# Optimization experiments

Measured on AMD Instinct MI355X. Metric: run time of the kernel, lower is better.

## Reference

```python
import jax, jax.numpy as jnp
import numpy as np

B, S, IN, H, OUT, L = 64, 2048, 208, 100, 98, 2


def setup_inputs() -> dict:
    key = jax.random.key(0)
    ks = jax.random.split(key, 11)
    sc = 1.0 / np.sqrt(H)  # pytorch GRU init scale
    return {
        "sequence": jax.random.normal(ks[0], (B, S, IN), jnp.float32),
        "h0": jnp.zeros((L, B, H), jnp.float32),
        "w_ih_l0": jax.random.normal(ks[1], (3 * H, IN), jnp.float32) * sc,
        "w_hh_l0": jax.random.normal(ks[2], (3 * H, H), jnp.float32) * sc,
        "b_ih_l0": jax.random.normal(ks[3], (3 * H,), jnp.float32) * sc,
        "b_hh_l0": jax.random.normal(ks[4], (3 * H,), jnp.float32) * sc,
        "w_ih_l1": jax.random.normal(ks[5], (3 * H, H), jnp.float32) * sc,
        "w_hh_l1": jax.random.normal(ks[6], (3 * H, H), jnp.float32) * sc,
        "b_ih_l1": jax.random.normal(ks[7], (3 * H,), jnp.float32) * sc,
        "b_hh_l1": jax.random.normal(ks[8], (3 * H,), jnp.float32) * sc,
        "w_out": jax.random.normal(ks[9], (OUT, H), jnp.float32) * sc,
        "b_out": jax.random.normal(ks[10], (OUT,), jnp.float32) * sc,
    }


def _gru_layer(x, h0, w_ih, w_hh, b_ih, b_hh):
    # x: (B,S,Din), h0: (B,H). PyTorch GRU gate order: r, z, n.
    Hd = h0.shape[-1]
    xg = jnp.einsum("bsi,gi->bsg", x, w_ih) + b_ih  # (B,S,3H) input projections, batched GEMM

    def step(h, xg_t):
        hg = h @ w_hh.T + b_hh  # (B,3H)
        xr, xz, xn = xg_t[:, :Hd], xg_t[:, Hd:2 * Hd], xg_t[:, 2 * Hd:]
        hr, hz, hn = hg[:, :Hd], hg[:, Hd:2 * Hd], hg[:, 2 * Hd:]
        r = jax.nn.sigmoid(xr + hr)
        z = jax.nn.sigmoid(xz + hz)
        n = jnp.tanh(xn + r * hn)
        h_new = (1.0 - z) * n + z * h
        return h_new, h_new

    h_last, ys = jax.lax.scan(step, h0, jnp.swapaxes(xg, 0, 1))  # scan over time
    return jnp.swapaxes(ys, 0, 1), h_last  # (B,S,H)


def reference(sequence, h0, w_ih_l0, w_hh_l0, b_ih_l0, b_hh_l0,
              w_ih_l1, w_hh_l1, b_ih_l1, b_hh_l1, w_out, b_out):
    # 2-layer unidirectional GRU (eval mode: inter-layer dropout inactive) + linear head
    y0, _ = _gru_layer(sequence, h0[0], w_ih_l0, w_hh_l0, b_ih_l0, b_hh_l0)
    y1, _ = _gru_layer(y0, h0[1], w_ih_l1, w_hh_l1, b_ih_l1, b_hh_l1)
    return jnp.einsum("bsh,oh->bso", y1, w_out) + b_out  # (B,S,OUT)
```

## Files before the change

kernel.cpp:

```cpp
#include <hip/hip_runtime.h>


#define GB_BM 64
#define GB_BN 64
#define GB_BK 16

__global__ __launch_bounds__(256)
void gemm_bias(const float* __restrict__ A, const float* __restrict__ W,
               const float* __restrict__ bias, float* __restrict__ C,
               int Sc, long a_bs, long a_ss, long c_bs, long c_ss,
               int N, int K)
{
    __shared__ float As[GB_BK][68];
    __shared__ float Bs[GB_BK][68];
    const int tid = threadIdx.x;
    const int m0 = blockIdx.x * GB_BM;
    const int n0 = blockIdx.y * GB_BN;

    const int lm = tid >> 2;
    const int lk = (tid & 3) << 2;
    const int row = m0 + lm;
    const float* arow = A + (long)(row / Sc) * a_bs + (long)(row % Sc) * a_ss;
    const int wrow = n0 + lm;
    const float* wrp = W + (long)wrow * K;
    const bool wv_ok = (wrow < N);

    const int tx = tid & 15;
    const int ty = tid >> 4;

    float acc[4][4] = {};

    for (int k0 = 0; k0 < K; k0 += GB_BK) {
        float4 av, bv;
        if (k0 + GB_BK <= K) {
            av = *(const float4*)(arow + k0 + lk);
            bv = wv_ok ? *(const float4*)(wrp + k0 + lk) : make_float4(0.f,0.f,0.f,0.f);
        } else {
            av = make_float4(0.f,0.f,0.f,0.f);
            bv = make_float4(0.f,0.f,0.f,0.f);
            const int kb = k0 + lk;
            if (kb + 0 < K) { av.x = arow[kb+0]; if (wv_ok) bv.x = wrp[kb+0]; }
            if (kb + 1 < K) { av.y = arow[kb+1]; if (wv_ok) bv.y = wrp[kb+1]; }
            if (kb + 2 < K) { av.z = arow[kb+2]; if (wv_ok) bv.z = wrp[kb+2]; }
            if (kb + 3 < K) { av.w = arow[kb+3]; if (wv_ok) bv.w = wrp[kb+3]; }
        }
        As[lk+0][lm] = av.x; As[lk+1][lm] = av.y; As[lk+2][lm] = av.z; As[lk+3][lm] = av.w;
        Bs[lk+0][lm] = bv.x; Bs[lk+1][lm] = bv.y; Bs[lk+2][lm] = bv.z; Bs[lk+3][lm] = bv.w;
        __syncthreads();
        #pragma unroll
        for (int kk = 0; kk < GB_BK; kk++) {
            float4 a  = *(const float4*)&As[kk][ty << 2];
            float4 bb = *(const float4*)&Bs[kk][tx << 2];
            float ar[4] = {a.x, a.y, a.z, a.w};
            float br[4] = {bb.x, bb.y, bb.z, bb.w};
            #pragma unroll
            for (int i = 0; i < 4; i++)
                #pragma unroll
                for (int j = 0; j < 4; j++)
                    acc[i][j] += ar[i] * br[j];
        }
        __syncthreads();
    }

    #pragma unroll
    for (int i = 0; i < 4; i++) {
        const int r = m0 + (ty << 2) + i;
        float* crow = C + (long)(r / Sc) * c_bs + (long)(r % Sc) * c_ss;
        #pragma unroll
        for (int j = 0; j < 4; j++) {
            const int col = n0 + (tx << 2) + j;
            if (col < N) crow[col] = acc[i][j] + bias[col];
        }
    }
}


#define RING_W 256
#define KPUB   16

__device__ __forceinline__ float fsig(float x)  { return 1.f / (1.f + __expf(-x)); }
__device__ __forceinline__ float ftanh(float x) { return 1.f - 2.f / (1.f + __expf(2.f * x)); }

__device__ __forceinline__ void bar_lgkm() {
    asm volatile("s_waitcnt lgkmcnt(0)" ::: "memory");
    __builtin_amdgcn_sched_barrier(0);
    __builtin_amdgcn_s_barrier();
}
__device__ __forceinline__ void bar_full() {
    asm volatile("s_waitcnt vmcnt(0) lgkmcnt(0)" ::: "memory");
    __builtin_amdgcn_sched_barrier(0);
    __builtin_amdgcn_s_barrier();
}

__device__ __forceinline__ void wait_ge(int* p, int tgt) {
    int spins = 0;
    while (__hip_atomic_load(p, __ATOMIC_ACQUIRE, __HIP_MEMORY_SCOPE_AGENT) < tgt) {
        __builtin_amdgcn_s_sleep(2);
        if (++spins > (1 << 22)) break;
    }
}

__global__ __launch_bounds__(640, 1)
void gru_fused(const float* __restrict__ xg0,
               const float* __restrict__ w_hh0, const float* __restrict__ b_hh0,
               const float* __restrict__ w_ih1, const float* __restrict__ b_ih1,
               const float* __restrict__ w_hh1, const float* __restrict__ b_hh1,
               const float* __restrict__ w_out, const float* __restrict__ b_out,
               const float* __restrict__ h_init,
               float* __restrict__ ring,
               int* prog0, int* cons1,
               float* __restrict__ out,
               int S)
{
    __shared__ __align__(16) float hs[100];
    __shared__ float hg_lds[300];
    __shared__ float xg_lds[300];

    const int tid   = threadIdx.x;
    const int layer = blockIdx.x >> 6;
    const int b     = blockIdx.x & 63;
    const int half  = tid & 1;
    const int g     = tid >> 1;
    const bool dot  = (tid < 600);
    const bool even = dot && (half == 0);

    int* myprog = prog0 + b * 32;
    int* mycons = cons1 + b * 32;

    float4 wv[13], wv2[13];
    float bhh = 0.f, bias2 = 0.f;
    const float* w_hh = layer ? w_hh1 : w_hh0;
    if (dot) {
        const float* p = w_hh + g * 100 + half * 48;
        #pragma unroll
        for (int i = 0; i < 13; i++) wv[i] = *(const float4*)(p + 4 * i);
        if (!half) wv[12] = make_float4(0.f, 0.f, 0.f, 0.f);
    }
    const bool has2 = layer == 0 ? dot : (tid < 196);
    if (has2) {
        const float* W2 = layer ? w_out : w_ih1;
        const float* p = W2 + g * 100 + half * 48;
        #pragma unroll
        for (int i = 0; i < 13; i++) wv2[i] = *(const float4*)(p + 4 * i);
        if (!half) wv2[12] = make_float4(0.f, 0.f, 0.f, 0.f);
    }
    if (even) bhh = (layer ? b_hh1 : b_hh0)[g];
    if (has2 && !half) bias2 = (layer ? b_out : b_ih1)[g];

    float hcur = 0.f;
    if (tid < 100) {
        hcur = h_init[layer * 6400 + b * 100 + tid];
        hs[tid] = hcur;
    }

    float* ringb = ring + (size_t)b * RING_W * 300;

    if (layer == 0) {
        const float* xgb = xg0 + (size_t)b * S * 300;
        float xnext = 0.f;
        if (even) xnext = xgb[g];
        __syncthreads();

        for (int t = 0; t < S; t++) {
            const float xcur = xnext;
            if (even && t + 1 < S) xnext = xgb[(size_t)(t + 1) * 300 + g];

            float tot = 0.f;
            if (dot) {
                const float4* hs4 = (const float4*)hs;
                const int base = half * 12;
                float a0 = 0.f, a1 = 0.f, a2 = 0.f, a3 = 0.f;
                #pragma unroll
                for (int i = 0; i < 13; i++) {
                    const float4 h4 = hs4[base + i];
                    const float4 w = wv[i];
                    a0 += w.x * h4.x; a1 += w.y * h4.y;
                    a2 += w.z * h4.z; a3 += w.w * h4.w;
                }
                tot = (a0 + a2) + (a1 + a3);
                tot += __shfl_down(tot, 1);
            }
            if (even) { hg_lds[g] = tot + bhh; xg_lds[g] = xcur; }
            if ((t & (KPUB - 1)) == 0) bar_full(); else bar_lgkm();

            if (tid == 0 && t > 0 && (t & (KPUB - 1)) == 0) {
                __hip_atomic_store(myprog, t, __ATOMIC_RELEASE, __HIP_MEMORY_SCOPE_AGENT);
                const int need = t + KPUB - RING_W;
                if (need > 0) wait_ge(mycons, need);
            }
            if (tid < 100) {
                const float xr = xg_lds[tid], xz = xg_lds[100 + tid], xn = xg_lds[200 + tid];
                const float hr = hg_lds[tid], hz = hg_lds[100 + tid], hn = hg_lds[200 + tid];
                const float r = fsig(xr + hr);
                const float z = fsig(xz + hz);
                const float n = ftanh(xn + r * hn);
                hcur = (1.f - z) * n + z * hcur;
                hs[tid] = hcur;
            }
            bar_lgkm();

            if (dot) {
                const float4* hs4 = (const float4*)hs;
                const int base = half * 12;
                float a0 = 0.f, a1 = 0.f, a2 = 0.f, a3 = 0.f;
                #pragma unroll
                for (int i = 0; i < 13; i++) {
                    const float4 h4 = hs4[base + i];
                    const float4 w = wv2[i];
                    a0 += w.x * h4.x; a1 += w.y * h4.y;
                    a2 += w.z * h4.z; a3 += w.w * h4.w;
                }
                float tot2 = (a0 + a2) + (a1 + a3);
                tot2 += __shfl_down(tot2, 1);
                if (!half) ringb[(size_t)(t & (RING_W - 1)) * 300 + g] = tot2 + bias2;
            }
        }
        bar_full();
        if (tid == 0)
            __hip_atomic_store(myprog, S, __ATOMIC_RELEASE, __HIP_MEMORY_SCOPE_AGENT);

    } else {
        float xnext = 0.f;
        if (tid == 0) {
            const int tgt0 = (KPUB + 1 < S) ? KPUB + 1 : S;
            wait_ge(myprog, tgt0);
        }
        __syncthreads();
        if (even) xnext = ringb[g];

        for (int t = 0; t < S; t++) {
            const float xcur = xnext;
            if (even && t + 1 < S)
                xnext = ringb[(size_t)((t + 1) & (RING_W - 1)) * 300 + g];

            float tot = 0.f;
            if (dot) {
                const float4* hs4 = (const float4*)hs;
                const int base = half * 12;
                float a0 = 0.f, a1 = 0.f, a2 = 0.f, a3 = 0.f;
                #pragma unroll
                for (int i = 0; i < 13; i++) {
                    const float4 h4 = hs4[base + i];
                    const float4 w = wv[i];
                    a0 += w.x * h4.x; a1 += w.y * h4.y;
                    a2 += w.z * h4.z; a3 += w.w * h4.w;
                }
                tot = (a0 + a2) + (a1 + a3);
                tot += __shfl_down(tot, 1);
            }
            if (even) { hg_lds[g] = tot + bhh; xg_lds[g] = xcur; }
            bar_lgkm();

            if (tid == 0) {
                if (t > 0 && (t & (KPUB - 1)) == 0)
                    __hip_atomic_store(mycons, t, __ATOMIC_RELEASE, __HIP_MEMORY_SCOPE_AGENT);
                if (((t + 1) & (KPUB - 1)) == 0) {
                    int tgt = t + 1 + KPUB + 1;
                    if (tgt > S) tgt = S;
                    wait_ge(myprog, tgt);
                }
            }
            if (tid < 100) {
                const float xr = xg_lds[tid], xz = xg_lds[100 + tid], xn = xg_lds[200 + tid];
                const float hr = hg_lds[tid], hz = hg_lds[100 + tid], hn = hg_lds[200 + tid];
                const float r = fsig(xr + hr);
                const float z = fsig(xz + hz);
                const float n = ftanh(xn + r * hn);
                hcur = (1.f - z) * n + z * hcur;
                hs[tid] = hcur;
            }
            bar_lgkm();

            if (tid < 196) {
                const float4* hs4 = (const float4*)hs;
                const int base = half * 12;
                float a0 = 0.f, a1 = 0.f, a2 = 0.f, a3 = 0.f;
                #pragma unroll
                for (int i = 0; i < 13; i++) {
                    const float4 h4 = hs4[base + i];
                    const float4 w = wv2[i];
                    a0 += w.x * h4.x; a1 += w.y * h4.y;
                    a2 += w.z * h4.z; a3 += w.w * h4.w;
                }
                float tot2 = (a0 + a2) + (a1 + a3);
                tot2 += __shfl_down(tot2, 1);
                if (!half) out[((size_t)b * S + t) * 98 + g] = tot2 + bias2;
            }
        }
    }
}


extern "C" void kernel_launch(void* const* d_in, const int* in_sizes, int n_in,
                              void* d_out, int out_size, void* d_ws, size_t ws_size,
                              hipStream_t stream)
{
    const float* seq    = (const float*)d_in[0];
    const float* h0     = (const float*)d_in[1];
    const float* w_ih0  = (const float*)d_in[2];
    const float* w_hh0  = (const float*)d_in[3];
    const float* b_ih0  = (const float*)d_in[4];
    const float* b_hh0  = (const float*)d_in[5];
    const float* w_ih1  = (const float*)d_in[6];
    const float* w_hh1  = (const float*)d_in[7];
    const float* b_ih1  = (const float*)d_in[8];
    const float* b_hh1  = (const float*)d_in[9];
    const float* w_out  = (const float*)d_in[10];
    const float* b_out  = (const float*)d_in[11];
    float* out = (float*)d_out;

    const int B = 64, S = 2048, IN = 208, G = 300;

    int* prog0 = (int*)d_ws;
    int* cons1 = prog0 + 64 * 32;
    float* xg0 = (float*)(cons1 + 64 * 32);
    float* ringbuf = xg0 + (size_t)B * S * G;

    hipMemsetAsync(d_ws, 0, 2 * 64 * 32 * sizeof(int), stream);

    const dim3 blk(256);
    const dim3 gX((B * S) / GB_BM, (G + GB_BN - 1) / GB_BN);
    gemm_bias<<<gX, blk, 0, stream>>>(seq, w_ih0, b_ih0, xg0,
                                      S, (long)S * IN, (long)IN,
                                      (long)S * G, (long)G, G, IN);

    gru_fused<<<dim3(128), dim3(640), 0, stream>>>(
        xg0, w_hh0, b_hh0, w_ih1, b_ih1, w_hh1, b_hh1, w_out, b_out,
        h0, ringbuf, prog0, cons1, out, S);
}
```

Before: 2.805 ms.

## Use intra-wave shuffles for gate exchange and double-buffer hidden state to drop a barrier

Rows are remapped so each hidden unit's r, z and n dot products sit in adjacent lanes of the same wavefront. Gates are then combined with __shfl instead of an LDS round trip and a barrier. The hidden state is double-buffered, and the second projection (w_ih1 or w_out) for step t-1 is computed in the same phase as step t's recurrence, which leaves one barrier per step instead of two. Launch bounds change to allow 3 blocks per CU. In exchange the producer/consumer sync logic is reshuffled with an offset ring write index, and some lanes do redundant clamped work.

```diff
diff --git a/kernel.cpp b/kernel.cpp
--- a/kernel.cpp
+++ b/kernel.cpp
@@ -91,7 +91,6 @@
     __builtin_amdgcn_sched_barrier(0);
     __builtin_amdgcn_s_barrier();
 }
-
 __device__ __forceinline__ void wait_ge(int* p, int tgt) {
     int spins = 0;
     while (__hip_atomic_load(p, __ATOMIC_ACQUIRE, __HIP_MEMORY_SCOPE_AGENT) < tgt) {
@@ -100,7 +99,7 @@
     }
 }
 
-__global__ __launch_bounds__(640, 1)
+__global__ __launch_bounds__(640, 3)
 void gru_fused(const float* __restrict__ xg0,
                const float* __restrict__ w_hh0, const float* __restrict__ b_hh0,
                const float* __restrict__ w_ih1, const float* __restrict__ b_ih1,
@@ -112,181 +111,178 @@
                float* __restrict__ out,
                int S)
 {
-    __shared__ __align__(16) float hs[100];
-    __shared__ float hg_lds[300];
-    __shared__ float xg_lds[300];
+    __shared__ __align__(16) float hs[2][104];
 
     const int tid   = threadIdx.x;
     const int layer = blockIdx.x >> 6;
     const int b     = blockIdx.x & 63;
-    const int half  = tid & 1;
-    const int g     = tid >> 1;
-    const bool dot  = (tid < 600);
-    const bool even = dot && (half == 0);
+
+    const int lane  = tid & 63;
+    const int wid   = tid >> 6;
+    const int pair  = lane >> 1;
+    const int jl    = pair / 3;
+    const int role  = pair - 3 * jl;
+    const int halfd = tid & 1;
+    const int j     = wid * 10 + jl;
+    const bool d1   = (lane < 60);
+    const bool evenl= d1 && (halfd == 0);
+    const bool gate = evenl && (role == 0);
+    const bool loadA= evenl && (role <= 1);
+    const int jc    = (j < 100) ? j : 99;
+    const int row1  = role * 100 + jc;
+
+    const int g2    = tid >> 1;
+    const int n2    = layer ? 98 : 300;
+    const bool act2 = (g2 < n2);
+    const int g2c   = act2 ? g2 : 0;
 
     int* myprog = prog0 + b * 32;
     int* mycons = cons1 + b * 32;
 
+    const float* w_hh = layer ? w_hh1 : w_hh0;
+    const float* W2   = layer ? w_out : w_ih1;
+
     float4 wv[13], wv2[13];
-    float bhh = 0.f, bias2 = 0.f;
-    const float* w_hh = layer ? w_hh1 : w_hh0;
-    if (dot) {
-        const float* p = w_hh + g * 100 + half * 48;
+    {
+        const float* p = w_hh + row1 * 100 + halfd * 48;
         #pragma unroll
         for (int i = 0; i < 13; i++) wv[i] = *(const float4*)(p + 4 * i);
-        if (!half) wv[12] = make_float4(0.f, 0.f, 0.f, 0.f);
-    }
-    const bool has2 = layer == 0 ? dot : (tid < 196);
-    if (has2) {
-        const float* W2 = layer ? w_out : w_ih1;
-        const float* p = W2 + g * 100 + half * 48;
-        #pragma unroll
-        for (int i = 0; i < 13; i++) wv2[i] = *(const float4*)(p + 4 * i);
-        if (!half) wv2[12] = make_float4(0.f, 0.f, 0.f, 0.f);
-    }
-    if (even) bhh = (layer ? b_hh1 : b_hh0)[g];
-    if (has2 && !half) bias2 = (layer ? b_out : b_ih1)[g];
+        if (!halfd) wv[12] = make_float4(0.f, 0.f, 0.f, 0.f);
+        const float* q = W2 + g2c * 100 + halfd * 48;
+        #pragma unroll
+        for (int i = 0; i < 13; i++) wv2[i] = *(const float4*)(q + 4 * i);
+        if (!halfd) wv2[12] = make_float4(0.f, 0.f, 0.f, 0.f);
+    }
+    const float bhh   = (layer ? b_hh1 : b_hh0)[row1];
+    const float bias2 = (layer ? b_out : b_ih1)[g2c];
 
     float hcur = 0.f;
-    if (tid < 100) {
-        hcur = h_init[layer * 6400 + b * 100 + tid];
-        hs[tid] = hcur;
-    }
-
-    float* ringb = ring + (size_t)b * RING_W * 300;
+    if (gate) hcur = h_init[layer * 6400 + b * 100 + j];
+    if (tid < 100) hs[0][tid] = h_init[layer * 6400 + b * 100 + tid];
+
+    float* ringb      = ring + (size_t)b * RING_W * 300;
+    const float* xgb  = xg0 + (size_t)b * (size_t)S * 300;
+    float* outb       = out + (size_t)b * (size_t)S * 98;
+
+    float xA_n = 0.f, xN_n = 0.f;
 
     if (layer == 0) {
-        const float* xgb = xg0 + (size_t)b * S * 300;
-        float xnext = 0.f;
-        if (even) xnext = xgb[g];
-        __syncthreads();
-
-        for (int t = 0; t < S; t++) {
-            const float xcur = xnext;
-            if (even && t + 1 < S) xnext = xgb[(size_t)(t + 1) * 300 + g];
-
-            float tot = 0.f;
-            if (dot) {
-                const float4* hs4 = (const float4*)hs;
-                const int base = half * 12;
-                float a0 = 0.f, a1 = 0.f, a2 = 0.f, a3 = 0.f;
-                #pragma unroll
-                for (int i = 0; i < 13; i++) {
-                    const float4 h4 = hs4[base + i];
-                    const float4 w = wv[i];
-                    a0 += w.x * h4.x; a1 += w.y * h4.y;
-                    a2 += w.z * h4.z; a3 += w.w * h4.w;
+        if (loadA) xA_n = xgb[row1];
+        if (gate)  xN_n = xgb[200 + j];
+    } else {
+        if (tid == 0) wait_ge(myprog, (S < KPUB + 1) ? S : (KPUB + 1));
+    }
+    __syncthreads();
+    if (layer == 1) {
+        if (loadA) xA_n = ringb[row1];
+        if (gate)  xN_n = ringb[200 + j];
+    }
+
+    for (int t = 0; t < S; t++) {
+        const int cur = t & 1;
+        const int nxt = cur ^ 1;
+        const float xA = xA_n, xN = xN_n;
+
+        if (t + 1 < S) {
+            const float* src = (layer == 0)
+                ? xgb + (size_t)(t + 1) * 300
+                : ringb + (size_t)((t + 1) & (RING_W - 1)) * 300;
+            if (loadA) xA_n = src[row1];
+            if (gate)  xN_n = src[200 + j];
+        }
+
+        const float4* h4p = (const float4*)hs[cur];
+        const int base = halfd * 12;
+        float a0 = 0.f, a1 = 0.f, a2 = 0.f, a3 = 0.f;
+        #pragma unroll
+        for (int i = 0; i < 13; i++) {
+            const float4 h4 = h4p[base + i];
+            const float4 w = wv[i];
+            a0 += w.x * h4.x; a1 += w.y * h4.y;
+            a2 += w.z * h4.z; a3 += w.w * h4.w;
+        }
+        float tot = (a0 + a2) + (a1 + a3);
+        tot += __shfl_down(tot, 1);
+        float val = tot + bhh;
+        if (loadA) val += xA;
+        const float zpre = __shfl(val, lane + 2);
+        const float hnv  = __shfl(val, lane + 4);
+
+        if (gate) {
+            const float r = fsig(val);
+            const float z = fsig(zpre);
+            const float n = ftanh(xN + r * hnv);
+            hcur = (1.f - z) * n + z * hcur;
+            hs[nxt][j] = hcur;
+        }
+
+        if (act2 && t > 0) {
+            float c0 = 0.f, c1 = 0.f, c2 = 0.f, c3 = 0.f;
+            #pragma unroll
+            for (int i = 0; i < 13; i++) {
+                const float4 h4 = h4p[base + i];
+                const float4 w = wv2[i];
+                c0 += w.x * h4.x; c1 += w.y * h4.y;
+                c2 += w.z * h4.z; c3 += w.w * h4.w;
+            }
+            float tot2 = (c0 + c2) + (c1 + c3);
+            tot2 += __shfl_down(tot2, 1);
+            if (!halfd) {
+                if (layer == 0)
+                    ringb[(size_t)((t - 1) & (RING_W - 1)) * 300 + g2] = tot2 + bias2;
+                else
+                    outb[(size_t)(t - 1) * 98 + g2] = tot2 + bias2;
+            }
+        }
+
+        if (((t + 1) & (KPUB - 1)) == 0) {
+            if (layer == 0) {
+                bar_full();
+                if (tid == 0) {
+                    __hip_atomic_store(myprog, t, __ATOMIC_RELEASE, __HIP_MEMORY_SCOPE_AGENT);
+                    const int need = t - 240;
+                    if (need > 0) wait_ge(mycons, need);
                 }
-                tot = (a0 + a2) + (a1 + a3);
-                tot += __shfl_down(tot, 1);
-            }
-            if (even) { hg_lds[g] = tot + bhh; xg_lds[g] = xcur; }
-            if ((t & (KPUB - 1)) == 0) bar_full(); else bar_lgkm();
-
-            if (tid == 0 && t > 0 && (t & (KPUB - 1)) == 0) {
-                __hip_atomic_store(myprog, t, __ATOMIC_RELEASE, __HIP_MEMORY_SCOPE_AGENT);
-                const int need = t + KPUB - RING_W;
-                if (need > 0) wait_ge(mycons, need);
-            }
-            if (tid < 100) {
-                const float xr = xg_lds[tid], xz = xg_lds[100 + tid], xn = xg_lds[200 + tid];
-                const float hr = hg_lds[tid], hz = hg_lds[100 + tid], hn = hg_lds[200 + tid];
-                const float r = fsig(xr + hr);
-                const float z = fsig(xz + hz);
-                const float n = ftanh(xn + r * hn);
-                hcur = (1.f - z) * n + z * hcur;
-                hs[tid] = hcur;
-            }
+            } else {
+                if (tid == 0) {
+                    __hip_atomic_store(mycons, t, __ATOMIC_RELEASE, __HIP_MEMORY_SCOPE_AGENT);
+                    int tgt = t + 2 + KPUB;
+                    if (tgt > S) tgt = S;
+                    wait_ge(myprog, tgt);
+                }
+                bar_lgkm();
+            }
+        } else {
             bar_lgkm();
-
-            if (dot) {
-                const float4* hs4 = (const float4*)hs;
-                const int base = half * 12;
-                float a0 = 0.f, a1 = 0.f, a2 = 0.f, a3 = 0.f;
-                #pragma unroll
-                for (int i = 0; i < 13; i++) {
-                    const float4 h4 = hs4[base + i];
-                    const float4 w = wv2[i];
-                    a0 += w.x * h4.x; a1 += w.y * h4.y;
-                    a2 += w.z * h4.z; a3 += w.w * h4.w;
-                }
-                float tot2 = (a0 + a2) + (a1 + a3);
-                tot2 += __shfl_down(tot2, 1);
-                if (!half) ringb[(size_t)(t & (RING_W - 1)) * 300 + g] = tot2 + bias2;
-            }
-        }
+        }
+    }
+
+    {
+        const float4* h4p = (const float4*)hs[S & 1];
+        const int base = halfd * 12;
+        if (act2) {
+            float c0 = 0.f, c1 = 0.f, c2 = 0.f, c3 = 0.f;
+            #pragma unroll
+            for (int i = 0; i < 13; i++) {
+                const float4 h4 = h4p[base + i];
+                const float4 w = wv2[i];
+                c0 += w.x * h4.x; c1 += w.y * h4.y;
+                c2 += w.z * h4.z; c3 += w.w * h4.w;
+            }
+            float tot2 = (c0 + c2) + (c1 + c3);
+            tot2 += __shfl_down(tot2, 1);
+            if (!halfd) {
+                if (layer == 0)
+                    ringb[(size_t)((S - 1) & (RING_W - 1)) * 300 + g2] = tot2 + bias2;
+                else
+                    outb[(size_t)(S - 1) * 98 + g2] = tot2 + bias2;
+            }
+        }
+    }
+    if (layer == 0) {
         bar_full();
         if (tid == 0)
             __hip_atomic_store(myprog, S, __ATOMIC_RELEASE, __HIP_MEMORY_SCOPE_AGENT);
-
-    } else {
-        float xnext = 0.f;
-        if (tid == 0) {
-            const int tgt0 = (KPUB + 1 < S) ? KPUB + 1 : S;
-            wait_ge(myprog, tgt0);
-        }
-        __syncthreads();
-        if (even) xnext = ringb[g];
-
-        for (int t = 0; t < S; t++) {
-            const float xcur = xnext;
-            if (even && t + 1 < S)
-                xnext = ringb[(size_t)((t + 1) & (RING_W - 1)) * 300 + g];
-
-            float tot = 0.f;
-            if (dot) {
-                const float4* hs4 = (const float4*)hs;
-                const int base = half * 12;
-                float a0 = 0.f, a1 = 0.f, a2 = 0.f, a3 = 0.f;
-                #pragma unroll
-                for (int i = 0; i < 13; i++) {
-                    const float4 h4 = hs4[base + i];
-                    const float4 w = wv[i];
-                    a0 += w.x * h4.x; a1 += w.y * h4.y;
-                    a2 += w.z * h4.z; a3 += w.w * h4.w;
-                }
-                tot = (a0 + a2) + (a1 + a3);
-                tot += __shfl_down(tot, 1);
-            }
-            if (even) { hg_lds[g] = tot + bhh; xg_lds[g] = xcur; }
-            bar_lgkm();
-
-            if (tid == 0) {
-                if (t > 0 && (t & (KPUB - 1)) == 0)
-                    __hip_atomic_store(mycons, t, __ATOMIC_RELEASE, __HIP_MEMORY_SCOPE_AGENT);
-                if (((t + 1) & (KPUB - 1)) == 0) {
-                    int tgt = t + 1 + KPUB + 1;
-                    if (tgt > S) tgt = S;
-                    wait_ge(myprog, tgt);
-                }
-            }
-            if (tid < 100) {
-                const float xr = xg_lds[tid], xz = xg_lds[100 + tid], xn = xg_lds[200 + tid];
-                const float hr = hg_lds[tid], hz = hg_lds[100 + tid], hn = hg_lds[200 + tid];
-                const float r = fsig(xr + hr);
-                const float z = fsig(xz + hz);
-                const float n = ftanh(xn + r * hn);
-                hcur = (1.f - z) * n + z * hcur;
-                hs[tid] = hcur;
-            }
-            bar_lgkm();
-
-            if (tid < 196) {
-                const float4* hs4 = (const float4*)hs;
-                const int base = half * 12;
-                float a0 = 0.f, a1 = 0.f, a2 = 0.f, a3 = 0.f;
-                #pragma unroll
-                for (int i = 0; i < 13; i++) {
-                    const float4 h4 = hs4[base + i];
-                    const float4 w = wv2[i];
-                    a0 += w.x * h4.x; a1 += w.y * h4.y;
-                    a2 += w.z * h4.z; a3 += w.w * h4.w;
-                }
-                float tot2 = (a0 + a2) + (a1 + a3);
-                tot2 += __shfl_down(tot2, 1);
-                if (!half) out[((size_t)b * S + t) * 98 + g] = tot2 + bias2;
-            }
-        }
     }
 }
 
```

Measured after the change: 2.948 ms. 5.1% more time.

## Fuse output projection into next step's recurrent dot to drop a barrier

Applied to the files above, without the earlier changes.

The per-step second matvec (input projection for layer 1, or the output head for layer 0's consumer) is deferred by one timestep and computed in the same loop as the next recurrent matvec. Both share the same LDS reads of the hidden state. This removes one LDS pass and one block barrier per timestep on the serial critical path, and unifies the two layer code paths into one loop. The ring and output writes lag one step, so a final epilogue writes the last timestep. Layer 1 now runs the output dot on all 600 threads with clamped weight rows, which adds register pressure and wasted lanes.

```diff
diff --git a/kernel.cpp b/kernel.cpp
--- a/kernel.cpp
+++ b/kernel.cpp
@@ -91,7 +91,6 @@
     __builtin_amdgcn_sched_barrier(0);
     __builtin_amdgcn_s_barrier();
 }
-
 __device__ __forceinline__ void wait_ge(int* p, int tgt) {
     int spins = 0;
     while (__hip_atomic_load(p, __ATOMIC_ACQUIRE, __HIP_MEMORY_SCOPE_AGENT) < tgt) {
@@ -112,7 +111,7 @@
                float* __restrict__ out,
                int S)
 {
-    __shared__ __align__(16) float hs[100];
+    __shared__ __align__(16) float hs[104];
     __shared__ float hg_lds[300];
     __shared__ float xg_lds[300];
 
@@ -124,28 +123,33 @@
     const bool dot  = (tid < 600);
     const bool even = dot && (half == 0);
 
+    const int n2    = layer ? 98 : 300;
+    const bool has2 = dot && (g < n2);
+    const int g2c   = (dot && g < n2) ? g : 0;
+
     int* myprog = prog0 + b * 32;
     int* mycons = cons1 + b * 32;
 
+    const float* w_hh = layer ? w_hh1 : w_hh0;
+    const float* W2   = layer ? w_out : w_ih1;
+
     float4 wv[13], wv2[13];
     float bhh = 0.f, bias2 = 0.f;
-    const float* w_hh = layer ? w_hh1 : w_hh0;
     if (dot) {
         const float* p = w_hh + g * 100 + half * 48;
+        const float* q = W2 + g2c * 100 + half * 48;
         #pragma unroll
-        for (int i = 0; i < 13; i++) wv[i] = *(const float4*)(p + 4 * i);
-        if (!half) wv[12] = make_float4(0.f, 0.f, 0.f, 0.f);
-    }
-    const bool has2 = layer == 0 ? dot : (tid < 196);
-    if (has2) {
-        const float* W2 = layer ? w_out : w_ih1;
-        const float* p = W2 + g * 100 + half * 48;
-        #pragma unroll
-        for (int i = 0; i < 13; i++) wv2[i] = *(const float4*)(p + 4 * i);
-        if (!half) wv2[12] = make_float4(0.f, 0.f, 0.f, 0.f);
+        for (int i = 0; i < 13; i++) {
+            wv[i]  = *(const float4*)(p + 4 * i);
+            wv2[i] = *(const float4*)(q + 4 * i);
+        }
+        if (!half) {
+            wv[12]  = make_float4(0.f, 0.f, 0.f, 0.f);
+            wv2[12] = make_float4(0.f, 0.f, 0.f, 0.f);
+        }
     }
     if (even) bhh = (layer ? b_hh1 : b_hh0)[g];
-    if (has2 && !half) bias2 = (layer ? b_out : b_ih1)[g];
+    if (even) bias2 = (layer ? b_out : b_ih1)[g2c];
 
     float hcur = 0.f;
     if (tid < 100) {
@@ -153,140 +157,114 @@
         hs[tid] = hcur;
     }
 
-    float* ringb = ring + (size_t)b * RING_W * 300;
+    float* ringb     = ring + (size_t)b * RING_W * 300;
+    const float* xgb = xg0 + (size_t)b * (size_t)S * 300;
+    float* outb      = out + (size_t)b * (size_t)S * 98;
+
+    float xnext = 0.f;
 
     if (layer == 0) {
-        const float* xgb = xg0 + (size_t)b * S * 300;
-        float xnext = 0.f;
         if (even) xnext = xgb[g];
-        __syncthreads();
-
-        for (int t = 0; t < S; t++) {
-            const float xcur = xnext;
-            if (even && t + 1 < S) xnext = xgb[(size_t)(t + 1) * 300 + g];
-
-            float tot = 0.f;
-            if (dot) {
-                const float4* hs4 = (const float4*)hs;
-                const int base = half * 12;
-                float a0 = 0.f, a1 = 0.f, a2 = 0.f, a3 = 0.f;
-                #pragma unroll
-                for (int i = 0; i < 13; i++) {
-                    const float4 h4 = hs4[base + i];
-                    const float4 w = wv[i];
-                    a0 += w.x * h4.x; a1 += w.y * h4.y;
-                    a2 += w.z * h4.z; a3 += w.w * h4.w;
-                }
-                tot = (a0 + a2) + (a1 + a3);
-                tot += __shfl_down(tot, 1);
+    } else {
+        if (tid == 0) wait_ge(myprog, (S < KPUB + 1) ? S : (KPUB + 1));
+    }
+    __syncthreads();
+    if (layer == 1 && even) xnext = ringb[g];
+
+    for (int t = 0; t < S; t++) {
+        const float xcur = xnext;
+        if (even && t + 1 < S) {
+            xnext = (layer == 0)
+                ? xgb[(size_t)(t + 1) * 300 + g]
+                : ringb[(size_t)((t + 1) & (RING_W - 1)) * 300 + g];
+        }
+
+        float tot = 0.f, tot2 = 0.f;
+        if (dot) {
+            const float4* hs4 = (const float4*)hs;
+            const int base = half * 12;
+            float a0 = 0.f, a1 = 0.f, a2 = 0.f, a3 = 0.f;
+            float c0 = 0.f, c1 = 0.f, c2 = 0.f, c3 = 0.f;
+            #pragma unroll
+            for (int i = 0; i < 13; i++) {
+                const float4 h4 = hs4[base + i];
+                const float4 w = wv[i];
+                const float4 u = wv2[i];
+                a0 += w.x * h4.x; a1 += w.y * h4.y;
+                a2 += w.z * h4.z; a3 += w.w * h4.w;
+                c0 += u.x * h4.x; c1 += u.y * h4.y;
+                c2 += u.z * h4.z; c3 += u.w * h4.w;
             }
-            if (even) { hg_lds[g] = tot + bhh; xg_lds[g] = xcur; }
+            tot = (a0 + a2) + (a1 + a3);
+            tot += __shfl_down(tot, 1);
+            tot2 = (c0 + c2) + (c1 + c3);
+            tot2 += __shfl_down(tot2, 1);
+        }
+        if (even) { hg_lds[g] = tot + bhh; xg_lds[g] = xcur; }
+
+        if (even && has2 && t > 0) {
+            if (layer == 0)
+                ringb[(size_t)((t - 1) & (RING_W - 1)) * 300 + g] = tot2 + bias2;
+            else
+                outb[(size_t)(t - 1) * 98 + g] = tot2 + bias2;
+        }
+
+        if (layer == 0) {
             if ((t & (KPUB - 1)) == 0) bar_full(); else bar_lgkm();
-
             if (tid == 0 && t > 0 && (t & (KPUB - 1)) == 0) {
                 __hip_atomic_store(myprog, t, __ATOMIC_RELEASE, __HIP_MEMORY_SCOPE_AGENT);
                 const int need = t + KPUB - RING_W;
                 if (need > 0) wait_ge(mycons, need);
             }
-            if (tid < 100) {
-                const float xr = xg_lds[tid], xz = xg_lds[100 + tid], xn = xg_lds[200 + tid];
-                const float hr = hg_lds[tid], hz = hg_lds[100 + tid], hn = hg_lds[200 + tid];
-                const float r = fsig(xr + hr);
-                const float z = fsig(xz + hz);
-                const float n = ftanh(xn + r * hn);
-                hcur = (1.f - z) * n + z * hcur;
-                hs[tid] = hcur;
-            }
+        } else {
             bar_lgkm();
-
-            if (dot) {
-                const float4* hs4 = (const float4*)hs;
-                const int base = half * 12;
-                float a0 = 0.f, a1 = 0.f, a2 = 0.f, a3 = 0.f;
-                #pragma unroll
-                for (int i = 0; i < 13; i++) {
-                    const float4 h4 = hs4[base + i];
-                    const float4 w = wv2[i];
-                    a0 += w.x * h4.x; a1 += w.y * h4.y;
-                    a2 += w.z * h4.z; a3 += w.w * h4.w;
-                }
-                float tot2 = (a0 + a2) + (a1 + a3);
-                tot2 += __shfl_down(tot2, 1);
-                if (!half) ringb[(size_t)(t & (RING_W - 1)) * 300 + g] = tot2 + bias2;
-            }
-        }
-        bar_full();
-        if (tid == 0)
-            __hip_atomic_store(myprog, S, __ATOMIC_RELEASE, __HIP_MEMORY_SCOPE_AGENT);
-
-    } else {
-        float xnext = 0.f;
-        if (tid == 0) {
-            const int tgt0 = (KPUB + 1 < S) ? KPUB + 1 : S;
-            wait_ge(myprog, tgt0);
-        }
-        __syncthreads();
-        if (even) xnext = ringb[g];
-
-        for (int t = 0; t < S; t++) {
-            const float xcur = xnext;
-            if (even && t + 1 < S)
-                xnext = ringb[(size_t)((t + 1) & (RING_W - 1)) * 300 + g];
-
-            float tot = 0.f;
-            if (dot) {
-                const float4* hs4 = (const float4*)hs;
-                const int base = half * 12;
-                float a0 = 0.f, a1 = 0.f, a2 = 0.f, a3 = 0.f;
-                #pragma unroll
-                for (int i = 0; i < 13; i++) {
-                    const float4 h4 = hs4[base + i];
-                    const float4 w = wv[i];
-                    a0 += w.x * h4.x; a1 += w.y * h4.y;
-                    a2 += w.z * h4.z; a3 += w.w * h4.w;
-                }
-                tot = (a0 + a2) + (a1 + a3);
-                tot += __shfl_down(tot, 1);
-            }
-            if (even) { hg_lds[g] = tot + bhh; xg_lds[g] = xcur; }
-            bar_lgkm();
-
             if (tid == 0) {
                 if (t > 0 && (t & (KPUB - 1)) == 0)
                     __hip_atomic_store(mycons, t, __ATOMIC_RELEASE, __HIP_MEMORY_SCOPE_AGENT);
                 if (((t + 1) & (KPUB - 1)) == 0) {
-                    int tgt = t + 1 + KPUB + 1;
+                    int tgt = t + 2 + KPUB;
                     if (tgt > S) tgt = S;
                     wait_ge(myprog, tgt);
                 }
             }
-            if (tid < 100) {
-                const float xr = xg_lds[tid], xz = xg_lds[100 + tid], xn = xg_lds[200 + tid];
-                const float hr = hg_lds[tid], hz = hg_lds[100 + tid], hn = hg_lds[200 + tid];
-                const float r = fsig(xr + hr);
-                const float z = fsig(xz + hz);
-                const float n = ftanh(xn + r * hn);
-                hcur = (1.f - z) * n + z * hcur;
-                hs[tid] = hcur;
-            }
-            bar_lgkm();
-
-            if (tid < 196) {
-                const float4* hs4 = (const float4*)hs;
-                const int base = half * 12;
-                float a0 = 0.f, a1 = 0.f, a2 = 0.f, a3 = 0.f;
-                #pragma unroll
-                for (int i = 0; i < 13; i++) {
-                    const float4 h4 = hs4[base + i];
-                    const float4 w = wv2[i];
-                    a0 += w.x * h4.x; a1 += w.y * h4.y;
-                    a2 += w.z * h4.z; a3 += w.w * h4.w;
-                }
-                float tot2 = (a0 + a2) + (a1 + a3);
-                tot2 += __shfl_down(tot2, 1);
-                if (!half) out[((size_t)b * S + t) * 98 + g] = tot2 + bias2;
-            }
-        }
+        }
+
+        if (tid < 100) {
+            const float xr = xg_lds[tid], xz = xg_lds[100 + tid], xn = xg_lds[200 + tid];
+            const float hr = hg_lds[tid], hz = hg_lds[100 + tid], hn = hg_lds[200 + tid];
+            const float r = fsig(xr + hr);
+            const float z = fsig(xz + hz);
+            const float n = ftanh(xn + r * hn);
+            hcur = (1.f - z) * n + z * hcur;
+            hs[tid] = hcur;
+        }
+        bar_lgkm();
+    }
+
+    if (dot) {
+        const float4* hs4 = (const float4*)hs;
+        const int base = half * 12;
+        float c0 = 0.f, c1 = 0.f, c2 = 0.f, c3 = 0.f;
+        #pragma unroll
+        for (int i = 0; i < 13; i++) {
+            const float4 h4 = hs4[base + i];
+            const float4 u = wv2[i];
+            c0 += u.x * h4.x; c1 += u.y * h4.y;
+            c2 += u.z * h4.z; c3 += u.w * h4.w;
+        }
+        float tot2 = (c0 + c2) + (c1 + c3);
+        tot2 += __shfl_down(tot2, 1);
+        if (even && has2) {
+            if (layer == 0)
+                ringb[(size_t)((S - 1) & (RING_W - 1)) * 300 + g] = tot2 + bias2;
+            else
+                outb[(size_t)(S - 1) * 98 + g] = tot2 + bias2;
+        }
+    }
+    if (layer == 0) {
+        bar_full();
+        if (tid == 0)
+            __hip_atomic_store(myprog, S, __ATOMIC_RELEASE, __HIP_MEMORY_SCOPE_AGENT);
     }
 }
 
```

Result: faster. 2.465 ms (-12.2%).
